# Kernel tuning notes

Measured on AMD Instinct MI355X. Metric: run time of the kernel, lower is better.

The kernel has to match this reference:

```python
import jax, jax.numpy as jnp
import numpy as np
import math

NUM_LAYERS = 2
NUM_HEADS = 8
D_MODEL = 256
D_FF = 4 * D_MODEL
FACTOR = 5
B, L, F_IN = 8, 2048, 32


def layer_norm(x, g, b, eps=1e-5):
    m = x.mean(-1, keepdims=True)
    v = ((x - m) ** 2).mean(-1, keepdims=True)
    return (x - m) * jax.lax.rsqrt(v + eps) * g + b


def prob_attention(q, k, v, idx):
    # q,k,v: [B,H,L,Dh]; idx: [L,S] sampled key indices per query (ProbSparse)
    Bq, H, Lq, Dh = q.shape
    u = min(FACTOR * math.ceil(math.log(Lq)), Lq)  # number of 'active' queries
    k_s = k[:, :, idx, :]                              # [B,H,L,S,Dh] gathered keys
    qk_s = jnp.einsum('bhld,bhlsd->bhls', q, k_s)      # sampled scores
    M = qk_s.max(-1) - qk_s.sum(-1) / Lq               # sparsity measure [B,H,L]
    _, top = jax.lax.top_k(M, u)                       # [B,H,u] active query idx
    q_red = jnp.take_along_axis(q, top[..., None], axis=2)   # [B,H,u,Dh]
    scores = jnp.einsum('bhud,bhld->bhul', q_red, k) * (1.0 / math.sqrt(Dh))
    attn = jax.nn.softmax(scores, axis=-1)             # [B,H,u,L]
    upd = jnp.einsum('bhul,bhld->bhud', attn, v)       # [B,H,u,Dh]
    # initial context = mean of V (mask_flag=False), then scatter active rows
    ctx = jnp.broadcast_to(v.mean(2, keepdims=True), (Bq, H, Lq, Dh))
    bi = jnp.arange(Bq)[:, None, None]
    hi = jnp.arange(H)[None, :, None]
    return ctx.at[bi, hi, top].set(upd)


def setup_inputs() -> dict:
    key = jax.random.key(0)
    ks = jax.random.split(key, 16)
    S = min(FACTOR * math.ceil(math.log(L)), L)  # 40
    std = 0.02

    def w(k, shape):
        return jax.random.normal(k, shape, jnp.float32) * std

    inp = {}
    inp['x'] = jax.random.normal(ks[0], (B, L, F_IN), jnp.float32)
    inp['idx_sample'] = jax.random.randint(ks[1], (NUM_LAYERS, L, S), 0, L)
    inp['w_in'] = w(ks[2], (F_IN, D_MODEL)); inp['b_in'] = jnp.zeros((D_MODEL,), jnp.float32)
    inp['wq'] = w(ks[3], (NUM_LAYERS, D_MODEL, D_MODEL)); inp['bq'] = jnp.zeros((NUM_LAYERS, D_MODEL), jnp.float32)
    inp['wk'] = w(ks[4], (NUM_LAYERS, D_MODEL, D_MODEL)); inp['bk'] = jnp.zeros((NUM_LAYERS, D_MODEL), jnp.float32)
    inp['wv'] = w(ks[5], (NUM_LAYERS, D_MODEL, D_MODEL)); inp['bv'] = jnp.zeros((NUM_LAYERS, D_MODEL), jnp.float32)
    inp['wo'] = w(ks[6], (NUM_LAYERS, D_MODEL, D_MODEL)); inp['bo'] = jnp.zeros((NUM_LAYERS, D_MODEL), jnp.float32)
    inp['w_ff1'] = w(ks[7], (NUM_LAYERS, D_MODEL, D_FF)); inp['b_ff1'] = jnp.zeros((NUM_LAYERS, D_FF), jnp.float32)
    inp['w_ff2'] = w(ks[8], (NUM_LAYERS, D_FF, D_MODEL)); inp['b_ff2'] = jnp.zeros((NUM_LAYERS, D_MODEL), jnp.float32)
    inp['ln1_g'] = jnp.ones((NUM_LAYERS, D_MODEL), jnp.float32); inp['ln1_b'] = jnp.zeros((NUM_LAYERS, D_MODEL), jnp.float32)
    inp['ln2_g'] = jnp.ones((NUM_LAYERS, D_MODEL), jnp.float32); inp['ln2_b'] = jnp.zeros((NUM_LAYERS, D_MODEL), jnp.float32)
    inp['w_fc1'] = w(ks[9], (D_MODEL, 64)); inp['b_fc1'] = jnp.zeros((64,), jnp.float32)
    inp['w_fc2'] = w(ks[10], (64, 1)); inp['b_fc2'] = jnp.zeros((1,), jnp.float32)
    return inp


def reference(x, idx_sample, w_in, b_in, wq, bq, wk, bk, wv, bv, wo, bo,
              w_ff1, b_ff1, w_ff2, b_ff2, ln1_g, ln1_b, ln2_g, ln2_b,
              w_fc1, b_fc1, w_fc2, b_fc2):
    Bx, Lx, _ = x.shape
    h = x @ w_in + b_in  # [B,L,D_MODEL]
    for i in range(NUM_LAYERS):
        q = (h @ wq[i] + bq[i]).reshape(Bx, Lx, NUM_HEADS, -1).transpose(0, 2, 1, 3)
        k = (h @ wk[i] + bk[i]).reshape(Bx, Lx, NUM_HEADS, -1).transpose(0, 2, 1, 3)
        v = (h @ wv[i] + bv[i]).reshape(Bx, Lx, NUM_HEADS, -1).transpose(0, 2, 1, 3)
        ctx = prob_attention(q, k, v, idx_sample[i])            # [B,H,L,Dh]
        ctx = ctx.transpose(0, 2, 1, 3).reshape(Bx, Lx, D_MODEL)
        new_x = ctx @ wo[i] + bo[i]
        h = layer_norm(h + new_x, ln1_g[i], ln1_b[i])
        y = jax.nn.relu(h @ w_ff1[i] + b_ff1[i]) @ w_ff2[i] + b_ff2[i]
        h = layer_norm(h + y, ln2_g[i], ln2_b[i])
    last = h[:, -1, :]                      # take final time step
    out = jax.nn.relu(last @ w_fc1 + b_fc1) @ w_fc2 + b_fc2
    return out[:, None, :]                  # unsqueeze(1) -> [B,1,output_size]
```

## Files before the change

### kernel.cpp

```cpp
#include <hip/hip_runtime.h>
#include <math.h>

#define BB 8
#define LL 2048
#define DM 256
#define NH 8
#define DH 32
#define DFF 1024
#define SS 40
#define UU 40
#define BL (BB*LL)
#define NSL 8

typedef unsigned short ushort_t;
typedef unsigned char uchar_t;
typedef __attribute__((ext_vector_type(8))) short short8;
typedef __attribute__((ext_vector_type(4))) float f32x4;

__device__ inline ushort_t f2b(float f)
{
    unsigned int u = __float_as_uint(f);
    u += 0x7fff + ((u >> 16) & 1);
    return (ushort_t)(u >> 16);
}

__device__ inline void gload16(const void* g, const void* l)
{
    __builtin_amdgcn_global_load_lds(
        (const __attribute__((address_space(1))) unsigned int*)g,
        (__attribute__((address_space(3))) unsigned int*)l, 16, 0, 0);
}

template<int RELU, int OUT_MODE>
__global__ __launch_bounds__(256)
void gemm_mfma(const ushort_t* __restrict__ A, const ushort_t* __restrict__ Bt,
               const float* __restrict__ bias, void* __restrict__ Cout,
               void* __restrict__ aux, int M, int N, int K)
{
    __shared__ ushort_t Asl[128 * 32];
    __shared__ ushort_t Bsl[128 * 32];

    const int t    = threadIdx.x;
    const int lane = t & 63;
    const int wv   = t >> 6;
    const int row0 = blockIdx.x * 128;
    const int col0 = blockIdx.y * 128;
    const int wr   = (wv >> 1) * 64;
    const int wc   = (wv & 1) * 64;
    const int quad = lane >> 4;
    const int l16  = lane & 15;

    f32x4 acc[4][4];
    #pragma unroll
    for (int i = 0; i < 4; ++i)
        #pragma unroll
        for (int j = 0; j < 4; ++j)
            acc[i][j] = 0.f;

    for (int k0 = 0; k0 < K; k0 += 32) {
        __syncthreads();
        #pragma unroll
        for (int r = 0; r < 2; ++r) {
            int g = r * 256 + t;
            const ushort_t* ga = A  + (size_t)(row0 + (g >> 2)) * K + k0 + (g & 3) * 8;
            const ushort_t* gb = Bt + (size_t)(col0 + (g >> 2)) * K + k0 + (g & 3) * 8;
            int lbase = (r * 256 + wv * 64) * 16;
            gload16(ga, (const char*)Asl + lbase);
            gload16(gb, (const char*)Bsl + lbase);
        }
        __syncthreads();

        short8 af[4], bfr[4];
        #pragma unroll
        for (int mi = 0; mi < 4; ++mi)
            af[mi] = *(const short8*)&Asl[(wr + mi * 16 + l16) * 32 + quad * 8];
        #pragma unroll
        for (int ni = 0; ni < 4; ++ni)
            bfr[ni] = *(const short8*)&Bsl[(wc + ni * 16 + l16) * 32 + quad * 8];
        #pragma unroll
        for (int mi = 0; mi < 4; ++mi)
            #pragma unroll
            for (int ni = 0; ni < 4; ++ni)
                acc[mi][ni] = __builtin_amdgcn_mfma_f32_16x16x32_bf16(
                    af[mi], bfr[ni], acc[mi][ni], 0, 0, 0);
    }

    #pragma unroll
    for (int mi = 0; mi < 4; ++mi) {
        #pragma unroll
        for (int ni = 0; ni < 4; ++ni) {
            int col = col0 + wc + ni * 16 + l16;
            float bb = bias[col];
            #pragma unroll
            for (int r = 0; r < 4; ++r) {
                int row = row0 + wr + mi * 16 + quad * 4 + r;
                float v = acc[mi][ni][r] + bb;
                if (RELU) v = v > 0.f ? v : 0.f;
                if (OUT_MODE == 0) {
                    ((float*)Cout)[(size_t)row * N + col] = v;
                } else if (OUT_MODE == 1) {
                    int tensor = col >> 8;
                    int c2 = col & 255;
                    int b  = row >> 11, l = row & (LL - 1);
                    int hh = c2 >> 5,  dh = c2 & 31;
                    int bh = b * NH + hh;
                    size_t bi = (((size_t)bh * LL + l) << 5) + dh;
                    ((float*)Cout)[(size_t)tensor * (BB*NH*LL*DH) + bi] = v;
                    if (tensor == 1)
                        ((ushort_t*)aux)[(((size_t)l << 6) + bh) * 32 + dh] = f2b(v);
                } else if (OUT_MODE == 2) {
                    ((ushort_t*)Cout)[(size_t)row * N + col] = f2b(v);
                } else {
                    ((float*)Cout)[(size_t)row * N + col] = v;
                    ((ushort_t*)aux)[(size_t)row * N + col] = f2b(v);
                }
            }
        }
    }
}

template<int HEAD>
__global__ __launch_bounds__(256)
void gemmln_k(const ushort_t* __restrict__ A, const ushort_t* __restrict__ Bt,
              const float* __restrict__ bias, float* __restrict__ h,
              ushort_t* __restrict__ hb, const float* __restrict__ g,
              const float* __restrict__ beta, int K,
              const float* __restrict__ w1, const float* __restrict__ b1,
              const float* __restrict__ w2, const float* __restrict__ b2,
              float* __restrict__ out)
{
    __shared__ ushort_t Asl[32 * 32];
    __shared__ ushort_t Bsl[256 * 32];
    __shared__ float rs[4][32], rs2[4][32];
    __shared__ float hrowS[256];

    const int t    = threadIdx.x;
    const int lane = t & 63;
    const int wv   = t >> 6;
    const int row0 = blockIdx.x * 32;
    const int wc   = wv * 64;
    const int quad = lane >> 4;
    const int l16  = lane & 15;

    f32x4 acc[2][4];
    #pragma unroll
    for (int i = 0; i < 2; ++i)
        #pragma unroll
        for (int j = 0; j < 4; ++j)
            acc[i][j] = 0.f;

    for (int k0 = 0; k0 < K; k0 += 32) {
        __syncthreads();
        if (wv < 2) {
            const ushort_t* ga = A + (size_t)(row0 + (t >> 2)) * K + k0 + (t & 3) * 8;
            gload16(ga, (const char*)Asl + wv * 1024);
        }
        #pragma unroll
        for (int r = 0; r < 4; ++r) {
            int gg = r * 256 + t;
            const ushort_t* gb = Bt + (size_t)(gg >> 2) * K + k0 + (gg & 3) * 8;
            gload16(gb, (const char*)Bsl + (r * 256 + wv * 64) * 16);
        }
        __syncthreads();

        short8 af[2], bfr[4];
        #pragma unroll
        for (int mi = 0; mi < 2; ++mi)
            af[mi] = *(const short8*)&Asl[(mi * 16 + l16) * 32 + quad * 8];
        #pragma unroll
        for (int ni = 0; ni < 4; ++ni)
            bfr[ni] = *(const short8*)&Bsl[(wc + ni * 16 + l16) * 32 + quad * 8];
        #pragma unroll
        for (int mi = 0; mi < 2; ++mi)
            #pragma unroll
            for (int ni = 0; ni < 4; ++ni)
                acc[mi][ni] = __builtin_amdgcn_mfma_f32_16x16x32_bf16(
                    af[mi], bfr[ni], acc[mi][ni], 0, 0, 0);
    }

    float gcol[4], bcol[4];
    #pragma unroll
    for (int ni = 0; ni < 4; ++ni) {
        int col = wc + ni * 16 + l16;
        gcol[ni] = g[col];
        bcol[ni] = beta[col];
    }
    float ps[2][4], ps2[2][4];
    #pragma unroll
    for (int mi = 0; mi < 2; ++mi) {
        #pragma unroll
        for (int r = 0; r < 4; ++r) {
            int row = row0 + mi * 16 + quad * 4 + r;
            float s = 0.f, s2 = 0.f;
            #pragma unroll
            for (int ni = 0; ni < 4; ++ni) {
                int col = wc + ni * 16 + l16;
                float v = acc[mi][ni][r] + bias[col] + h[(size_t)row * DM + col];
                acc[mi][ni][r] = v;
                s += v;
                s2 += v * v;
            }
            ps[mi][r] = s;
            ps2[mi][r] = s2;
        }
    }
    #pragma unroll
    for (int off = 1; off < 16; off <<= 1) {
        #pragma unroll
        for (int mi = 0; mi < 2; ++mi)
            #pragma unroll
            for (int r = 0; r < 4; ++r) {
                ps[mi][r]  += __shfl_xor(ps[mi][r],  off, 16);
                ps2[mi][r] += __shfl_xor(ps2[mi][r], off, 16);
            }
    }
    if (l16 == 0) {
        #pragma unroll
        for (int mi = 0; mi < 2; ++mi)
            #pragma unroll
            for (int r = 0; r < 4; ++r) {
                int lrow = mi * 16 + quad * 4 + r;
                rs[wv][lrow]  = ps[mi][r];
                rs2[wv][lrow] = ps2[mi][r];
            }
    }
    __syncthreads();

    #pragma unroll
    for (int mi = 0; mi < 2; ++mi) {
        #pragma unroll
        for (int r = 0; r < 4; ++r) {
            int lrow = mi * 16 + quad * 4 + r;
            int row  = row0 + lrow;
            float tot  = rs[0][lrow] + rs[1][lrow] + rs[2][lrow] + rs[3][lrow];
            float tot2 = rs2[0][lrow] + rs2[1][lrow] + rs2[2][lrow] + rs2[3][lrow];
            float mean = tot * (1.f / (float)DM);
            float var  = tot2 * (1.f / (float)DM) - mean * mean;
            float inv  = 1.0f / sqrtf(var + 1e-5f);
            #pragma unroll
            for (int ni = 0; ni < 4; ++ni) {
                int col = wc + ni * 16 + l16;
                float val = (acc[mi][ni][r] - mean) * inv * gcol[ni] + bcol[ni];
                h[(size_t)row * DM + col]  = val;
                hb[(size_t)row * DM + col] = f2b(val);
                if (HEAD && lrow == 31) hrowS[col] = val;
            }
        }
    }

    if (HEAD) {
        __syncthreads();
        if ((blockIdx.x & 63) == 63 && t < 64) {
            int b = blockIdx.x >> 6;
            float s = 0.f;
            for (int kk = 0; kk < DM; ++kk)
                s = fmaf(hrowS[kk], w1[kk * 64 + t], s);
            s += b1[t];
            s = s > 0.f ? s : 0.f;
            float contrib = s * w2[t];
            #pragma unroll
            for (int off = 32; off > 0; off >>= 1)
                contrib += __shfl_down(contrib, off, 64);
            if (t == 0) out[b] = contrib + b2[0];
        }
    }
}

__device__ inline void tcvt_dev(float (*tile)[33], const float* __restrict__ src,
                                ushort_t* __restrict__ dst, int K, int N,
                                int matStride, int bi)
{
    int tilesN = N >> 5;
    int tpm = (K >> 5) * tilesN;
    int m   = bi / tpm;
    int tid = bi % tpm;
    int k0 = (tid / tilesN) << 5, n0 = (tid % tilesN) << 5;
    const float* s = src + (size_t)m * K * N;
    ushort_t*    d = dst + (size_t)m * matStride;
    int r = threadIdx.x >> 5, c = threadIdx.x & 31;
    #pragma unroll
    for (int i = 0; i < 4; ++i)
        tile[r + 8 * i][c] = s[(size_t)(k0 + r + 8 * i) * N + n0 + c];
    __syncthreads();
    #pragma unroll
    for (int i = 0; i < 4; ++i)
        d[(size_t)(n0 + r + 8 * i) * K + k0 + c] = f2b(tile[c][r + 8 * i]);
}

__global__ __launch_bounds__(256)
void preproc_k(const float* __restrict__ wq, const float* __restrict__ wk,
               const float* __restrict__ wv, const float* __restrict__ wo,
               const float* __restrict__ wf1, const float* __restrict__ wf2,
               const float* __restrict__ w_in,
               const float* __restrict__ bq, const float* __restrict__ bk,
               const float* __restrict__ bv, const float* __restrict__ x,
               ushort_t* __restrict__ wqkvT, ushort_t* __restrict__ woT,
               ushort_t* __restrict__ wf1T, ushort_t* __restrict__ wf2T,
               ushort_t* __restrict__ w_inT, float* __restrict__ bqkv,
               ushort_t* __restrict__ xb16)
{
    __shared__ float tile[32][33];
    int b = blockIdx.x;
    if (b < 512) {
        int which = b >> 7, lb = b & 127;
        const float* src = which == 0 ? wq : which == 1 ? wk : which == 2 ? wv : wo;
        ushort_t* dst = which == 0 ? wqkvT : which == 1 ? wqkvT + 65536
                       : which == 2 ? wqkvT + 131072 : woT;
        int stride = which == 3 ? 65536 : 768 * 256;
        tcvt_dev(tile, src, dst, DM, DM, stride, lb);
    } else if (b < 1024) {
        tcvt_dev(tile, wf1, wf1T, DM, DFF, 1024 * 256, b - 512);
    } else if (b < 1536) {
        tcvt_dev(tile, wf2, wf2T, DFF, DM, 256 * 1024, b - 1024);
    } else if (b < 1544) {
        tcvt_dev(tile, w_in, w_inT, 32, DM, 256 * 32, b - 1536);
    } else if (b < 1550) {
        int t = (b - 1544) * 256 + threadIdx.x;
        int i = t / 768, j = t % 768;
        const float* s = j < 256 ? bq : (j < 512 ? bk : bv);
        bqkv[t] = s[i * 256 + (j & 255)];
    } else {
        int tid = (b - 1550) * 256 + threadIdx.x;
        float4 v = ((const float4*)x)[tid];
        unsigned int lo = f2b(v.x) | ((unsigned int)f2b(v.y) << 16);
        unsigned int hi = f2b(v.z) | ((unsigned int)f2b(v.w) << 16);
        ((uint2*)xb16)[tid] = make_uint2(lo, hi);
    }
}

__global__ __launch_bounds__(256)
void metric2_k(const float* __restrict__ qb, const ushort_t* __restrict__ kT,
               const int* __restrict__ idx, float* __restrict__ Mout,
               unsigned int* __restrict__ jidx32)
{
    __shared__ float mst[64][5];
    int t = threadIdx.x;
    int w = t >> 6, lane = t & 63;
    int l = blockIdx.x * 4 + w;

    if (t < 64) {
        int zb = t >> 3, sel = t & 7;
        int zl = blockIdx.x * 4 + (sel >> 1), half = sel & 1;
        jidx32[(size_t)(zb * LL + zl) * 2 + half] = 0;
    }

    const float4* qr = (const float4*)(qb + ((size_t)(lane * LL + l) << 5));
    float4 q[8];
    #pragma unroll
    for (int i = 0; i < 8; ++i) q[i] = qr[i];

    int r40 = idx[l * SS + (lane < SS ? lane : SS - 1)];

    float mx = -3e38f, sm = 0.f;
    for (int s = 0; s < SS; ++s) {
        int r = __shfl(r40, s, 64);
        const uint4* kr = (const uint4*)(kT + (((size_t)r << 6) + lane) * 32);
        float d = 0.f;
        #pragma unroll
        for (int ww = 0; ww < 4; ++ww) {
            uint4 kv = kr[ww];
            float4 qa = q[2 * ww], qb2 = q[2 * ww + 1];
            d = fmaf(__uint_as_float(kv.x << 16),         qa.x, d);
            d = fmaf(__uint_as_float(kv.x & 0xffff0000u), qa.y, d);
            d = fmaf(__uint_as_float(kv.y << 16),         qa.z, d);
            d = fmaf(__uint_as_float(kv.y & 0xffff0000u), qa.w, d);
            d = fmaf(__uint_as_float(kv.z << 16),         qb2.x, d);
            d = fmaf(__uint_as_float(kv.z & 0xffff0000u), qb2.y, d);
            d = fmaf(__uint_as_float(kv.w << 16),         qb2.z, d);
            d = fmaf(__uint_as_float(kv.w & 0xffff0000u), qb2.w, d);
        }
        mx = fmaxf(mx, d);
        sm += d;
    }
    mst[lane][w] = mx - sm * (1.0f / (float)LL);
    __syncthreads();

    int bh = t >> 2, ls = t & 3;
    Mout[(size_t)bh * LL + blockIdx.x * 4 + ls] = mst[bh][ls];
}

__global__ __launch_bounds__(512)
void topkf_k(const float* __restrict__ Mout, int* __restrict__ top,
             uchar_t* __restrict__ jidx)
{
    __shared__ float cvS[320];
    __shared__ int   ciS[320];
    int bh = blockIdx.x;
    int t  = threadIdx.x;
    int lane = t & 63, w = t >> 6;
    int l0 = w << 8;

    float v[4];
    #pragma unroll
    for (int i = 0; i < 4; ++i)
        v[i] = Mout[(size_t)bh * LL + l0 + i * 64 + lane];

    for (int r = 0; r < UU; ++r) {
        float bv = -3e38f; int bi = 1 << 30;
        #pragma unroll
        for (int i = 0; i < 4; ++i) {
            int idx = l0 + i * 64 + lane;
            if (v[i] > bv || (v[i] == bv && idx < bi)) { bv = v[i]; bi = idx; }
        }
        #pragma unroll
        for (int off = 32; off > 0; off >>= 1) {
            float ov = __shfl_down(bv, off, 64);
            int   oi = __shfl_down(bi, off, 64);
            if (ov > bv || (ov == bv && oi < bi)) { bv = ov; bi = oi; }
        }
        bv = __shfl(bv, 0, 64);
        bi = __shfl(bi, 0, 64);
        if (lane == 0) { cvS[w * UU + r] = bv; ciS[w * UU + r] = bi; }
        int rel = bi - l0;
        if ((rel & 63) == lane) v[rel >> 6] = -3e38f;
    }
    __syncthreads();

    for (int c = t; c < 320; c += 512) {
        float mv = cvS[c]; int mi = ciS[c];
        int rank = 0;
        for (int j = 0; j < 320; ++j)
            rank += (cvS[j] > mv) || (cvS[j] == mv && ciS[j] < mi);
        if (rank < UU) {
            top[bh * UU + rank] = mi;
            int b = bh >> 3, hh = bh & 7;
            jidx[(size_t)(b * LL + mi) * 8 + hh] = (uchar_t)(rank + 1);
        }
    }
}

__global__ __launch_bounds__(256)
void attnupd_k(const float* __restrict__ qb, const float* __restrict__ kb,
               const float* __restrict__ vb, const int* __restrict__ top,
               float* __restrict__ mP, float* __restrict__ sP,
               float* __restrict__ OP, float* __restrict__ vmeanP)
{
    __shared__ float qs[UU * 32];
    __shared__ float sc[UU * 256];
    __shared__ float msh[UU];

    int blk = blockIdx.x;
    int sl  = blk & (NSL - 1);
    int bh  = blk >> 3;
    int t   = threadIdx.x;
    int l0  = sl << 8;

    for (int i = t; i < UU * 32; i += 256) {
        int j = i >> 5, dd = i & 31;
        qs[i] = qb[((size_t)(bh * LL + top[bh * UU + j]) << 5) + dd];
    }

    const float4* kr = (const float4*)(kb + ((size_t)(bh * LL + l0 + t) << 5));
    float4 k4[8];
    #pragma unroll
    for (int i = 0; i < 8; ++i) k4[i] = kr[i];
    __syncthreads();

    const float scale = 0.17677669529663687f;
    #pragma unroll 4
    for (int j = 0; j < UU; ++j) {
        float ds = 0.f;
        #pragma unroll
        for (int i = 0; i < 8; ++i) {
            float4 qv = *(const float4*)&qs[j * 32 + 4 * i];
            ds = fmaf(qv.x, k4[i].x, ds);
            ds = fmaf(qv.y, k4[i].y, ds);
            ds = fmaf(qv.z, k4[i].z, ds);
            ds = fmaf(qv.w, k4[i].w, ds);
        }
        sc[j * 256 + t] = ds * scale;
    }
    __syncthreads();

    int j8 = t >> 5, d = t & 31;
    #pragma unroll
    for (int g = 0; g < 5; ++g) {
        int j = g * 8 + j8;
        float4 a = *(const float4*)&sc[j * 256 + 4 * d];
        float4 b = *(const float4*)&sc[j * 256 + 128 + 4 * d];
        float m = fmaxf(fmaxf(fmaxf(a.x, a.y), fmaxf(a.z, a.w)),
                        fmaxf(fmaxf(b.x, b.y), fmaxf(b.z, b.w)));
        #pragma unroll
        for (int off = 16; off > 0; off >>= 1)
            m = fmaxf(m, __shfl_down(m, off, 64));
        if (d == 0) msh[j] = m;
    }
    __syncthreads();

    #pragma unroll 8
    for (int i = t; i < UU * 256; i += 256) {
        int j = i >> 8;
        sc[i] = __expf(sc[i] - msh[j]);
    }
    __syncthreads();

    int pq = bh * NSL + sl;

    #pragma unroll
    for (int g = 0; g < 5; ++g) {
        int j = g * 8 + j8;
        float4 a = *(const float4*)&sc[j * 256 + 4 * d];
        float4 b = *(const float4*)&sc[j * 256 + 128 + 4 * d];
        float s = a.x + a.y + a.z + a.w + b.x + b.y + b.z + b.w;
        #pragma unroll
        for (int off = 16; off > 0; off >>= 1)
            s += __shfl_down(s, off, 64);
        if (d == 0) { sP[pq * UU + j] = s; mP[pq * UU + j] = msh[j]; }
    }

    const float* vbase = vb + ((size_t)(bh * LL + l0) << 5) + d;
    float acc[5] = {0.f, 0.f, 0.f, 0.f, 0.f};
    float vsum = 0.f;
    #pragma unroll 4
    for (int i = 0; i < 64; ++i) {
        float v0 = vbase[(4 * i + 0) << 5];
        float v1 = vbase[(4 * i + 1) << 5];
        float v2 = vbase[(4 * i + 2) << 5];
        float v3 = vbase[(4 * i + 3) << 5];
        vsum += v0 + v1 + v2 + v3;
        #pragma unroll
        for (int g = 0; g < 5; ++g) {
            float4 e4 = *(const float4*)&sc[(g * 8 + j8) * 256 + 4 * i];
            acc[g] = fmaf(e4.x, v0, acc[g]);
            acc[g] = fmaf(e4.y, v1, acc[g]);
            acc[g] = fmaf(e4.z, v2, acc[g]);
            acc[g] = fmaf(e4.w, v3, acc[g]);
        }
    }
    #pragma unroll
    for (int g = 0; g < 5; ++g)
        OP[((size_t)pq * UU + g * 8 + j8) * 32 + d] = acc[g];
    if (j8 == 0) vmeanP[pq * 32 + d] = vsum;
}

__global__ __launch_bounds__(256)
void fillcomb_k(const float* __restrict__ vmeanP, const uchar_t* __restrict__ jidx,
                const float* __restrict__ mP, const float* __restrict__ sP,
                const float* __restrict__ OP, ushort_t* __restrict__ ctxb)
{
    int tid = blockIdx.x * 256 + threadIdx.x;
    int pr   = tid & 127;
    int rowi = tid >> 7;
    int b    = rowi >> 11;
    int hh   = pr >> 4;
    int bh   = b * 8 + hh;
    int d0   = (pr * 2) & 31;
    int j    = (int)jidx[(size_t)rowi * 8 + hh];

    float v0, v1;
    if (j == 0) {
        float s0 = 0.f, s1 = 0.f;
        #pragma unroll
        for (int q = 0; q < NSL; ++q) {
            s0 += vmeanP[(bh * NSL + q) * 32 + d0];
            s1 += vmeanP[(bh * NSL + q) * 32 + d0 + 1];
        }
        v0 = s0 * (1.f / (float)LL);
        v1 = s1 * (1.f / (float)LL);
    } else {
        int jj = j - 1;
        float M = -3e38f;
        #pragma unroll
        for (int q = 0; q < NSL; ++q) M = fmaxf(M, mP[(bh * NSL + q) * UU + jj]);
        float S = 0.f, O0 = 0.f, O1 = 0.f;
        #pragma unroll
        for (int q = 0; q < NSL; ++q) {
            float wgt = __expf(mP[(bh * NSL + q) * UU + jj] - M);
            S  = fmaf(sP[(bh * NSL + q) * UU + jj], wgt, S);
            O0 = fmaf(OP[((size_t)(bh * NSL + q) * UU + jj) * 32 + d0], wgt, O0);
            O1 = fmaf(OP[((size_t)(bh * NSL + q) * UU + jj) * 32 + d0 + 1], wgt, O1);
        }
        v0 = O0 / S;
        v1 = O1 / S;
    }
    ((unsigned int*)ctxb)[tid] = (unsigned int)f2b(v0) | ((unsigned int)f2b(v1) << 16);
}

extern "C" void kernel_launch(void* const* d_in, const int* in_sizes, int n_in,
                              void* d_out, int out_size, void* d_ws, size_t ws_size,
                              hipStream_t stream)
{
    const float* x    = (const float*)d_in[0];
    const int*   idx  = (const int*)  d_in[1];
    const float* w_in = (const float*)d_in[2];
    const float* b_in = (const float*)d_in[3];
    const float* wq   = (const float*)d_in[4];
    const float* bq   = (const float*)d_in[5];
    const float* wk   = (const float*)d_in[6];
    const float* bk   = (const float*)d_in[7];
    const float* wv   = (const float*)d_in[8];
    const float* bv   = (const float*)d_in[9];
    const float* wo   = (const float*)d_in[10];
    const float* bo   = (const float*)d_in[11];
    const float* wf1  = (const float*)d_in[12];
    const float* bf1  = (const float*)d_in[13];
    const float* wf2  = (const float*)d_in[14];
    const float* bf2  = (const float*)d_in[15];
    const float* g1   = (const float*)d_in[16];
    const float* be1  = (const float*)d_in[17];
    const float* g2   = (const float*)d_in[18];
    const float* be2  = (const float*)d_in[19];
    const float* wfc1 = (const float*)d_in[20];
    const float* bfc1 = (const float*)d_in[21];
    const float* wfc2 = (const float*)d_in[22];
    const float* bfc2 = (const float*)d_in[23];
    float* out = (float*)d_out;

    float* ws = (float*)d_ws;
    float*    h     = ws;
    float*    qkv   = ws + 4194304;
    float*    qb    = qkv;
    float*    kb    = qkv + 4194304;
    float*    vb    = qkv + 8388608;
    float*    attnS = ws + 16777216;
    ushort_t* kT16  = (ushort_t*)attnS;
    float*    Mbuf  = attnS + 2097152;
    float*    vmeP  = attnS + 2269184;
    float*    OP    = attnS + 2285568;
    float*    mP    = attnS + 2940928;
    float*    sP    = attnS + 2961408;
    uchar_t*  jidx  = (uchar_t*)(attnS + 2981888);
    float*    scr   = ws + 20971520;
    ushort_t* xb16  = (ushort_t*)scr;
    int*      top   = (int*)(scr + 264192);
    ushort_t* hb    = (ushort_t*)(scr + 266752);
    ushort_t* wqkvT = (ushort_t*)(scr + 2363904);
    ushort_t* woT   = (ushort_t*)(scr + 2560512);
    ushort_t* wf1T  = (ushort_t*)(scr + 2626048);
    ushort_t* wf2T  = (ushort_t*)(scr + 2888192);
    ushort_t* w_inT = (ushort_t*)(scr + 3150336);
    float*    bqkv  = scr + 3154432;
    ushort_t* ctxb  = (ushort_t*)qkv;
    ushort_t* ffbb  = (ushort_t*)(qkv + 2097152);

    dim3 blk(256);

    preproc_k<<<dim3(2062), blk, 0, stream>>>(
        wq, wk, wv, wo, wf1, wf2, w_in, bq, bk, bv, x,
        wqkvT, woT, wf1T, wf2T, w_inT, bqkv, xb16);

    gemm_mfma<0,3><<<dim3(BL/128, 2), blk, 0, stream>>>(
        xb16, w_inT, b_in, (void*)h, (void*)hb, BL, DM, 32);

    for (int i = 0; i < 2; ++i) {
        gemm_mfma<0,1><<<dim3(BL/128, 6), blk, 0, stream>>>(
            hb, wqkvT + (size_t)i*768*256, bqkv + i*768, (void*)qkv, (void*)kT16,
            BL, 768, DM);

        metric2_k<<<dim3(512), blk, 0, stream>>>(
            qb, kT16, idx + (size_t)i*LL*SS, Mbuf, (unsigned int*)jidx);
        topkf_k<<<dim3(BB*NH), dim3(512), 0, stream>>>(Mbuf, top, jidx);
        attnupd_k<<<dim3(BB*NH*NSL), blk, 0, stream>>>(qb, kb, vb, top, mP, sP, OP, vmeP);
        fillcomb_k<<<dim3(BL*DM/512), blk, 0, stream>>>(vmeP, jidx, mP, sP, OP, ctxb);

        gemmln_k<0><<<dim3(BL/32), blk, 0, stream>>>(
            ctxb, woT + (size_t)i*256*256, bo + i*DM, h, hb,
            g1 + i*DM, be1 + i*DM, DM,
            nullptr, nullptr, nullptr, nullptr, nullptr);

        gemm_mfma<1,2><<<dim3(BL/128, 8), blk, 0, stream>>>(
            hb, wf1T + (size_t)i*1024*256, bf1 + i*DFF, (void*)ffbb, nullptr, BL, DFF, DM);

        if (i == 1) {
            gemmln_k<1><<<dim3(BL/32), blk, 0, stream>>>(
                ffbb, wf2T + (size_t)i*256*1024, bf2 + i*DM, h, hb,
                g2 + i*DM, be2 + i*DM, DFF,
                wfc1, bfc1, wfc2, bfc2, out);
        } else {
            gemmln_k<0><<<dim3(BL/32), blk, 0, stream>>>(
                ffbb, wf2T + (size_t)i*256*1024, bf2 + i*DM, h, hb,
                g2 + i*DM, be2 + i*DM, DFF,
                nullptr, nullptr, nullptr, nullptr, nullptr);
        }
    }
}
```

Measured before the change: 503.1 us.

## Use bf16 MFMA for sparse-attention score and PV products in attnupd_k

```diff
diff --git a/kernel.cpp b/kernel.cpp
--- a/kernel.cpp
+++ b/kernel.cpp
@@ -11,6 +11,10 @@
 #define UU 40
 #define BL (BB*LL)
 #define NSL 8
+
+#define SCP 260
+#define KP  40
+#define VP  34
 
 typedef unsigned short ushort_t;
 typedef unsigned char uchar_t;
@@ -435,40 +439,57 @@
                float* __restrict__ mP, float* __restrict__ sP,
                float* __restrict__ OP, float* __restrict__ vmeanP)
 {
-    __shared__ float qs[UU * 32];
-    __shared__ float sc[UU * 256];
-    __shared__ float msh[UU];
+    __shared__ ushort_t qs[48 * KP];
+    __shared__ ushort_t kv[256 * KP];
+    __shared__ float    sc[48 * SCP];
+    __shared__ float    msh[UU];
+    __shared__ float    red[8][32];
 
     int blk = blockIdx.x;
     int sl  = blk & (NSL - 1);
     int bh  = blk >> 3;
     int t   = threadIdx.x;
     int l0  = sl << 8;
-
-    for (int i = t; i < UU * 32; i += 256) {
+    int lane = t & 63, wvx = t >> 6;
+    int quad = lane >> 4, l16 = lane & 15;
+    const float scale = 0.17677669529663687f;
+
+    for (int i = t; i < 48 * 32; i += 256) {
         int j = i >> 5, dd = i & 31;
-        qs[i] = qb[((size_t)(bh * LL + top[bh * UU + j]) << 5) + dd];
-    }
-
-    const float4* kr = (const float4*)(kb + ((size_t)(bh * LL + l0 + t) << 5));
-    float4 k4[8];
-    #pragma unroll
-    for (int i = 0; i < 8; ++i) k4[i] = kr[i];
-    __syncthreads();
-
-    const float scale = 0.17677669529663687f;
-    #pragma unroll 4
-    for (int j = 0; j < UU; ++j) {
-        float ds = 0.f;
+        float v = (j < UU) ? qb[((size_t)(bh * LL + top[bh * UU + j]) << 5) + dd] : 0.f;
+        qs[j * KP + dd] = f2b(v);
+    }
+    {
+        const float4* kr = (const float4*)(kb + ((size_t)(bh * LL + l0 + t) << 5));
         #pragma unroll
         for (int i = 0; i < 8; ++i) {
-            float4 qv = *(const float4*)&qs[j * 32 + 4 * i];
-            ds = fmaf(qv.x, k4[i].x, ds);
-            ds = fmaf(qv.y, k4[i].y, ds);
-            ds = fmaf(qv.z, k4[i].z, ds);
-            ds = fmaf(qv.w, k4[i].w, ds);
-        }
-        sc[j * 256 + t] = ds * scale;
+            float4 kx = kr[i];
+            *(unsigned int*)&kv[t * KP + 4 * i] =
+                (unsigned int)f2b(kx.x) | ((unsigned int)f2b(kx.y) << 16);
+            *(unsigned int*)&kv[t * KP + 4 * i + 2] =
+                (unsigned int)f2b(kx.z) | ((unsigned int)f2b(kx.w) << 16);
+        }
+    }
+    __syncthreads();
+
+    {
+        short8 afq[3];
+        #pragma unroll
+        for (int mt = 0; mt < 3; ++mt)
+            afq[mt] = *(const short8*)&qs[(mt * 16 + l16) * KP + quad * 8];
+        #pragma unroll
+        for (int n4 = 0; n4 < 4; ++n4) {
+            int nt = wvx * 4 + n4;
+            short8 bk = *(const short8*)&kv[(nt * 16 + l16) * KP + quad * 8];
+            #pragma unroll
+            for (int mt = 0; mt < 3; ++mt) {
+                f32x4 dd = {0.f, 0.f, 0.f, 0.f};
+                dd = __builtin_amdgcn_mfma_f32_16x16x32_bf16(afq[mt], bk, dd, 0, 0, 0);
+                #pragma unroll
+                for (int r = 0; r < 4; ++r)
+                    sc[(mt * 16 + quad * 4 + r) * SCP + nt * 16 + l16] = dd[r] * scale;
+            }
+        }
     }
     __syncthreads();
 
@@ -476,8 +497,8 @@
     #pragma unroll
     for (int g = 0; g < 5; ++g) {
         int j = g * 8 + j8;
-        float4 a = *(const float4*)&sc[j * 256 + 4 * d];
-        float4 b = *(const float4*)&sc[j * 256 + 128 + 4 * d];
+        float4 a = *(const float4*)&sc[j * SCP + 4 * d];
+        float4 b = *(const float4*)&sc[j * SCP + 128 + 4 * d];
         float m = fmaxf(fmaxf(fmaxf(a.x, a.y), fmaxf(a.z, a.w)),
                         fmaxf(fmaxf(b.x, b.y), fmaxf(b.z, b.w)));
         #pragma unroll
@@ -487,10 +508,15 @@
     }
     __syncthreads();
 
-    #pragma unroll 8
-    for (int i = t; i < UU * 256; i += 256) {
-        int j = i >> 8;
-        sc[i] = __expf(sc[i] - msh[j]);
+    #pragma unroll 2
+    for (int i = t; i < UU * 64; i += 256) {
+        int j = i >> 6;
+        float* p = &sc[j * SCP + (i & 63) * 4];
+        float4 e = *(float4*)p;
+        float mm = msh[j];
+        e.x = __expf(e.x - mm); e.y = __expf(e.y - mm);
+        e.z = __expf(e.z - mm); e.w = __expf(e.w - mm);
+        *(float4*)p = e;
     }
     __syncthreads();
 
@@ -499,38 +525,72 @@
     #pragma unroll
     for (int g = 0; g < 5; ++g) {
         int j = g * 8 + j8;
-        float4 a = *(const float4*)&sc[j * 256 + 4 * d];
-        float4 b = *(const float4*)&sc[j * 256 + 128 + 4 * d];
+        float4 a = *(const float4*)&sc[j * SCP + 4 * d];
+        float4 b = *(const float4*)&sc[j * SCP + 128 + 4 * d];
         float s = a.x + a.y + a.z + a.w + b.x + b.y + b.z + b.w;
         #pragma unroll
         for (int off = 16; off > 0; off >>= 1)
             s += __shfl_down(s, off, 64);
         if (d == 0) { sP[pq * UU + j] = s; mP[pq * UU + j] = msh[j]; }
     }
-
-    const float* vbase = vb + ((size_t)(bh * LL + l0) << 5) + d;
-    float acc[5] = {0.f, 0.f, 0.f, 0.f, 0.f};
-    float vsum = 0.f;
-    #pragma unroll 4
-    for (int i = 0; i < 64; ++i) {
-        float v0 = vbase[(4 * i + 0) << 5];
-        float v1 = vbase[(4 * i + 1) << 5];
-        float v2 = vbase[(4 * i + 2) << 5];
-        float v3 = vbase[(4 * i + 3) << 5];
-        vsum += v0 + v1 + v2 + v3;
-        #pragma unroll
-        for (int g = 0; g < 5; ++g) {
-            float4 e4 = *(const float4*)&sc[(g * 8 + j8) * 256 + 4 * i];
-            acc[g] = fmaf(e4.x, v0, acc[g]);
-            acc[g] = fmaf(e4.y, v1, acc[g]);
-            acc[g] = fmaf(e4.z, v2, acc[g]);
-            acc[g] = fmaf(e4.w, v3, acc[g]);
-        }
-    }
-    #pragma unroll
-    for (int g = 0; g < 5; ++g)
-        OP[((size_t)pq * UU + g * 8 + j8) * 32 + d] = acc[g];
-    if (j8 == 0) vmeanP[pq * 32 + d] = vsum;
+    {
+        const float4* vr = (const float4*)(vb + ((size_t)(bh * LL + l0 + t) << 5));
+        #pragma unroll
+        for (int i = 0; i < 8; ++i) {
+            float4 vx = vr[i];
+            *(unsigned int*)&kv[t * VP + 4 * i] =
+                (unsigned int)f2b(vx.x) | ((unsigned int)f2b(vx.y) << 16);
+            *(unsigned int*)&kv[t * VP + 4 * i + 2] =
+                (unsigned int)f2b(vx.z) | ((unsigned int)f2b(vx.w) << 16);
+        }
+        const float* base = vb + ((size_t)(bh * LL + l0 + j8 * 32) << 5) + d;
+        float s = 0.f;
+        #pragma unroll 8
+        for (int i = 0; i < 32; ++i) s += base[(size_t)i << 5];
+        red[j8][d] = s;
+    }
+    __syncthreads();
+
+    if (t < 32) {
+        float tot = 0.f;
+        #pragma unroll
+        for (int p = 0; p < 8; ++p) tot += red[p][t];
+        vmeanP[pq * 32 + t] = tot;
+    }
+
+    if (wvx < 3) {
+        f32x4 acc0 = {0.f, 0.f, 0.f, 0.f};
+        f32x4 acc1 = {0.f, 0.f, 0.f, 0.f};
+        #pragma unroll
+        for (int ks = 0; ks < 8; ++ks) {
+            float4 p0 = *(const float4*)&sc[(wvx * 16 + l16) * SCP + ks * 32 + quad * 8];
+            float4 p1 = *(const float4*)&sc[(wvx * 16 + l16) * SCP + ks * 32 + quad * 8 + 4];
+            short8 af;
+            af[0] = (short)f2b(p0.x); af[1] = (short)f2b(p0.y);
+            af[2] = (short)f2b(p0.z); af[3] = (short)f2b(p0.w);
+            af[4] = (short)f2b(p1.x); af[5] = (short)f2b(p1.y);
+            af[6] = (short)f2b(p1.z); af[7] = (short)f2b(p1.w);
+            #pragma unroll
+            for (int nt = 0; nt < 2; ++nt) {
+                short8 bf;
+                #pragma unroll
+                for (int jj = 0; jj < 8; ++jj)
+                    bf[jj] = (short)kv[(ks * 32 + quad * 8 + jj) * VP + nt * 16 + l16];
+                if (nt == 0)
+                    acc0 = __builtin_amdgcn_mfma_f32_16x16x32_bf16(af, bf, acc0, 0, 0, 0);
+                else
+                    acc1 = __builtin_amdgcn_mfma_f32_16x16x32_bf16(af, bf, acc1, 0, 0, 0);
+            }
+        }
+        #pragma unroll
+        for (int r = 0; r < 4; ++r) {
+            int j = wvx * 16 + quad * 4 + r;
+            if (j < UU) {
+                OP[((size_t)pq * UU + j) * 32 + l16]      = acc0[r];
+                OP[((size_t)pq * UU + j) * 32 + 16 + l16] = acc1[r];
+            }
+        }
+    }
 }
 
 __global__ __launch_bounds__(256)
```

Measured after the change: 474.1 us. 5.8% less time.
